# Kernel tuning notes

Measured on AMD Instinct MI355X. Metric: run time of the kernel, lower is better.

Reference implementation:

```python
import jax, jax.numpy as jnp
import numpy as np

EPS = 1e-12  # torch F.normalize eps

def _colnorm(w, g):
    # F.normalize(w, dim=0, p=2) * g  (column-wise L2 over dim 0)
    n = jnp.sqrt(jnp.sum(w * w, axis=0, keepdims=True))
    return (w / jnp.maximum(n, EPS)) * g

def setup_inputs() -> dict:
    key = jax.random.key(0)
    ks = jax.random.split(key, 16)
    B, T, V, E, H = 16, 512, 8192, 512, 1024
    inp = {
        'xs': jax.random.randint(ks[0], (B, T), 0, V),
        'ys': jax.random.randint(ks[1], (B, T), 0, V),
        'embed_w': jax.random.normal(ks[2], (V, E), jnp.float32) * 0.02,
        'wx': jax.random.normal(ks[3], (E, 4 * H), jnp.float32),
        'wh': jax.random.normal(ks[4], (H, 4 * H), jnp.float32),
        'wmx': jax.random.normal(ks[5], (E, H), jnp.float32),
        'wmh': jax.random.normal(ks[6], (H, H), jnp.float32),
        'b': jax.random.normal(ks[7], (4 * H,), jnp.float32) * 0.02,
        'gx': jax.random.normal(ks[8], (4 * H,), jnp.float32),
        'gh': jax.random.normal(ks[9], (4 * H,), jnp.float32),
        'gmx': jax.random.normal(ks[10], (H,), jnp.float32),
        'gmh': jax.random.normal(ks[11], (H,), jnp.float32),
        'pred_w': jax.random.normal(ks[12], (V, H), jnp.float32) * 0.02,
        'pred_b': jax.random.normal(ks[13], (V,), jnp.float32) * 0.02,
    }
    return inp

def reference(xs, ys, embed_w, wx, wh, wmx, wmh, b, gx, gh, gmx, gmh, pred_w, pred_b):
    B, T = xs.shape
    H = wmh.shape[0]
    V = pred_w.shape[0]
    # padding_idx=0 -> embedding row 0 is zero
    ew = embed_w.at[0].set(0.0)
    x = ew[xs]  # [B, T, E]
    # weight norm
    wx_n = _colnorm(wx, gx)
    wh_n = _colnorm(wh, gh)
    wmx_n = _colnorm(wmx, gmx)
    wmh_n = _colnorm(wmh, gmh)
    # precompute input-dependent projections (same math, batched over time)
    zx = jnp.einsum('bte,ef->btf', x, wx_n) + b     # [B, T, 4H]
    mx = jnp.einsum('bte,eh->bth', x, wmx_n)        # [B, T, H]

    def step(carry, inp):
        h, c = carry
        zx_t, mx_t = inp
        m = mx_t * (h @ wmh_n)                       # [B, H]
        z = zx_t + m @ wh_n                          # [B, 4H]
        i, f, o, u = jnp.split(z, 4, axis=1)
        i = jax.nn.sigmoid(i)
        f = jax.nn.sigmoid(f)
        o = jax.nn.sigmoid(o)
        u = jnp.tanh(u)
        c = f * c + i * u
        h = o * jnp.tanh(c)
        return (h, c), h

    h0 = jnp.zeros((B, H), x.dtype)
    c0 = jnp.zeros((B, H), x.dtype)
    _, hs = jax.lax.scan(step, (h0, c0), (zx.transpose(1, 0, 2), mx.transpose(1, 0, 2)))
    hs = hs.transpose(1, 0, 2)  # [B, T, H]
    logits = jnp.einsum('bth,vh->btv', hs, pred_w) + pred_b
    log_p = jax.nn.log_softmax(logits.reshape(B * T, V), axis=-1)
    nll = -jnp.take_along_axis(log_p, ys.reshape(B * T, 1), axis=1)
    return jnp.mean(nll)
```

## Files before the change

kernel.cpp:

```cpp
#include <hip/hip_runtime.h>
#include <hip/hip_bf16.h>
#include <stdint.h>

#define B_   16
#define T_   512
#define V_   8192
#define E_   512
#define H_   1024
#define BT_  (B_ * T_)
#define H4_  (4 * H_)

typedef __attribute__((ext_vector_type(8))) short   short8;
typedef __attribute__((ext_vector_type(8))) __bf16  bf16x8;
typedef __attribute__((ext_vector_type(4))) float   f32x4;
typedef __attribute__((ext_vector_type(4))) short   short4v;
typedef unsigned long long ull;

__device__ __forceinline__ float bf2f(short s) {
  union { unsigned u; float f; } x;
  x.u = ((unsigned)(unsigned short)s) << 16;
  return x.f;
}
__device__ __forceinline__ short f2bf(float f) {
  union { float f; unsigned u; } x; x.f = f;
  unsigned u = x.u;
  u = (u + 0x7fffu + ((u >> 16) & 1u)) >> 16;
  return (short)u;
}
__device__ __forceinline__ f32x4 mfma16(short8 a, short8 b, f32x4 c) {
  return __builtin_amdgcn_mfma_f32_16x16x32_bf16(
      __builtin_bit_cast(bf16x8, a), __builtin_bit_cast(bf16x8, b), c, 0, 0, 0);
}
__device__ __forceinline__ float sigm(float x) { return 1.f / (1.f + __expf(-x)); }
__device__ __forceinline__ float tanh_f(float x) { return 1.f - 2.f / (__expf(2.f * x) + 1.f); }

__device__ __forceinline__ short8 mk8(ull lo, ull hi) {
  union { ull u[2]; short8 s; } c;
  c.u[0] = lo; c.u[1] = hi;
  return c.s;
}

__global__ __launch_bounds__(256) void colscale(const float* __restrict__ W,
                                                const float* __restrict__ g,
                                                float* __restrict__ sc, int Kr, int N) {
  int j = blockIdx.x * 256 + threadIdx.x;
  if (j >= N) return;
  float ss = 0.f;
  for (int i = 0; i < Kr; ++i) { float v = W[(long)i * N + j]; ss = fmaf(v, v, ss); }
  sc[j] = g[j] / fmaxf(sqrtf(ss), 1e-12f);
}

__global__ __launch_bounds__(256) void transpose_cast(const float* __restrict__ W,
                                                      const float* __restrict__ sc,
                                                      short* __restrict__ WT, int Kr, int N) {
  __shared__ float tile[32][33];
  int nbi = Kr >> 5;
  int bi = blockIdx.x % nbi, bj = blockIdx.x / nbi;
  int i0 = bi << 5, j0 = bj << 5;
  int tx = threadIdx.x & 31, ty = threadIdx.x >> 5;
  for (int yy = ty; yy < 32; yy += 8)
    tile[yy][tx] = W[(long)(i0 + yy) * N + j0 + tx];
  __syncthreads();
  for (int yy = ty; yy < 32; yy += 8) {
    int j = j0 + yy;
    WT[(long)j * Kr + i0 + tx] = f2bf(tile[tx][yy] * sc[j]);
  }
}

__global__ __launch_bounds__(256) void castbf(const float* __restrict__ src,
                                              short* __restrict__ dst, long n) {
  long i = ((long)blockIdx.x * 256 + threadIdx.x) * 4;
  if (i + 3 < n) {
    float4 v = *(const float4*)(src + i);
    short4v o = { f2bf(v.x), f2bf(v.y), f2bf(v.z), f2bf(v.w) };
    *(short4v*)(dst + i) = o;
  }
}

__global__ __launch_bounds__(256) void embed_gather(const int* __restrict__ xs,
                                                    const float* __restrict__ ew,
                                                    short* __restrict__ x) {
  int r = blockIdx.x;
  int idx = xs[r];
  const float* src = ew + (long)idx * E_;
  for (int e = threadIdx.x; e < E_; e += 256) {
    float v = (idx == 0) ? 0.f : src[e];
    x[(long)r * E_ + e] = f2bf(v);
  }
}

__global__ __launch_bounds__(256) void gemm_bt(const short* __restrict__ A,
                                               const short* __restrict__ BT,
                                               const float* __restrict__ bias,
                                               short* __restrict__ C,
                                               int M, int N, int K) {
  int ntiles = N >> 7;
  int tM = (blockIdx.x / ntiles) << 7;
  int tN = (blockIdx.x % ntiles) << 7;
  int w = threadIdx.x >> 6, lane = threadIdx.x & 63;
  int mo = tM + ((w & 1) << 6), no = tN + ((w >> 1) << 6);
  int lr = lane & 15, lk8 = (lane >> 4) << 3, q = lane >> 4;
  f32x4 acc[4][4] = {};
  const short* Ap = A + (long)(mo + lr) * K + lk8;
  const short* Bp = BT + (long)(no + lr) * K + lk8;
  for (int k0 = 0; k0 < K; k0 += 32) {
    short8 af[4], bfr[4];
#pragma unroll
    for (int i = 0; i < 4; ++i) af[i] = *(const short8*)(Ap + (long)16 * i * K + k0);
#pragma unroll
    for (int j = 0; j < 4; ++j) bfr[j] = *(const short8*)(Bp + (long)16 * j * K + k0);
#pragma unroll
    for (int i = 0; i < 4; ++i)
#pragma unroll
      for (int j = 0; j < 4; ++j)
        acc[i][j] = mfma16(af[i], bfr[j], acc[i][j]);
  }
  float pbv[4];
#pragma unroll
  for (int j = 0; j < 4; ++j) pbv[j] = bias ? bias[no + 16 * j + lr] : 0.f;
#pragma unroll
  for (int i = 0; i < 4; ++i)
#pragma unroll
    for (int j = 0; j < 4; ++j)
#pragma unroll
      for (int r = 0; r < 4; ++r) {
        int row = mo + 16 * i + 4 * q + r;
        int col = no + 16 * j + lr;
        C[(long)row * N + col] = f2bf(acc[i][j][r] + pbv[j]);
      }
}

__global__ __launch_bounds__(256) void gemm_logits(const short* __restrict__ A,
                                                   const short* __restrict__ BT,
                                                   const float* __restrict__ pb,
                                                   const int* __restrict__ ys,
                                                   float* __restrict__ sumexp,
                                                   float* __restrict__ logit_y,
                                                   int M, int N, int K) {
  int ntiles = N >> 7;
  int tM = (blockIdx.x / ntiles) << 7;
  int tN = (blockIdx.x % ntiles) << 7;
  int w = threadIdx.x >> 6, lane = threadIdx.x & 63;
  int mo = tM + ((w & 1) << 6), no = tN + ((w >> 1) << 6);
  int lr = lane & 15, lk8 = (lane >> 4) << 3, q = lane >> 4;
  f32x4 acc[4][4] = {};
  const short* Ap = A + (long)(mo + lr) * K + lk8;
  const short* Bp = BT + (long)(no + lr) * K + lk8;
  for (int k0 = 0; k0 < K; k0 += 32) {
    short8 af[4], bfr[4];
#pragma unroll
    for (int i = 0; i < 4; ++i) af[i] = *(const short8*)(Ap + (long)16 * i * K + k0);
#pragma unroll
    for (int j = 0; j < 4; ++j) bfr[j] = *(const short8*)(Bp + (long)16 * j * K + k0);
#pragma unroll
    for (int i = 0; i < 4; ++i)
#pragma unroll
      for (int j = 0; j < 4; ++j)
        acc[i][j] = mfma16(af[i], bfr[j], acc[i][j]);
  }
  float pbv[4];
#pragma unroll
  for (int j = 0; j < 4; ++j) pbv[j] = pb[no + 16 * j + lr];
#pragma unroll
  for (int i = 0; i < 4; ++i) {
#pragma unroll
    for (int r = 0; r < 4; ++r) {
      int row = mo + 16 * i + 4 * q + r;
      int ysr = ys[row];
      float s = 0.f;
#pragma unroll
      for (int j = 0; j < 4; ++j) {
        float v = acc[i][j][r] + pbv[j];
        s += __expf(v);
        int col = no + 16 * j + lr;
        if (col == ysr) logit_y[row] = v;
      }
      s += __shfl_xor(s, 1); s += __shfl_xor(s, 2);
      s += __shfl_xor(s, 4); s += __shfl_xor(s, 8);
      if (lr == 0) atomicAdd(&sumexp[row], s);
    }
  }
}

#define NWG_ 64

__global__ __launch_bounds__(256, 1) void scan_kernel(
    const short* __restrict__ zxb, const short* __restrict__ mxb,
    const short* __restrict__ wmhT, const short* __restrict__ whT,
    short* __restrict__ hs,
    ull* __restrict__ h_prev,
    ull* __restrict__ m_buf,
    unsigned* __restrict__ flags_m,
    unsigned* __restrict__ flags_h) {
  const int g = blockIdx.x;
  const int tid = threadIdx.x;
  const int w = tid >> 6, lane = tid & 63;
  const int lr = lane & 15, q = lane >> 4;
  const int colg = g << 4;
  const int b = tid >> 4, cl = tid & 15;

  __shared__ float red1[4][16][16];
  __shared__ float red2[4][4][16][16];
  __shared__ __align__(8) short mtile[16][16];
  __shared__ __align__(8) short htile[16][16];

  short8 wmh_f[8];
#pragma unroll
  for (int kk = 0; kk < 8; ++kk) {
    const ull* p = (const ull*)(wmhT + (long)(colg + lr) * H_ + (w << 8) + (kk << 5) + (q << 3));
    ull lo = __hip_atomic_load(p, __ATOMIC_RELAXED, __HIP_MEMORY_SCOPE_WORKGROUP);
    ull hi = __hip_atomic_load(p + 1, __ATOMIC_RELAXED, __HIP_MEMORY_SCOPE_WORKGROUP);
    wmh_f[kk] = mk8(lo, hi);
  }
  short8 wh_f[4][8];
#pragma unroll
  for (int gt = 0; gt < 4; ++gt)
#pragma unroll
    for (int kk = 0; kk < 8; ++kk) {
      const ull* p = (const ull*)(whT + (long)(gt * H_ + colg + lr) * H_ + (w << 8) + (kk << 5) + (q << 3));
      ull lo = __hip_atomic_load(p, __ATOMIC_RELAXED, __HIP_MEMORY_SCOPE_WORKGROUP);
      ull hi = __hip_atomic_load(p + 1, __ATOMIC_RELAXED, __HIP_MEMORY_SCOPE_WORKGROUP);
      wh_f[gt][kk] = mk8(lo, hi);
    }

  float c = 0.f;
  const ull* hp = h_prev + lr * 256 + (w << 6) + (q << 1);
  const ull* mp = m_buf + lr * 256 + (w << 6) + (q << 1);

  for (int t = 0; t < T_; ++t) {
    long rrow = (long)(b * T_ + t);
    short mx_p = mxb[rrow * H_ + colg + cl];
    const short* zrow = zxb + rrow * H4_ + colg + cl;
    short z0p = zrow[0 * H_], z1p = zrow[1 * H_], z2p = zrow[2 * H_], z3p = zrow[3 * H_];

    if (tid < NWG_)
      while (__hip_atomic_load(&flags_h[tid << 5], __ATOMIC_RELAXED,
                               __HIP_MEMORY_SCOPE_AGENT) < (unsigned)t) {}
    __syncthreads();

    ull lh[16];
#pragma unroll
    for (int kk = 0; kk < 8; ++kk) {
      lh[2 * kk]     = __hip_atomic_load(hp + (kk << 3),     __ATOMIC_RELAXED, __HIP_MEMORY_SCOPE_AGENT);
      lh[2 * kk + 1] = __hip_atomic_load(hp + (kk << 3) + 1, __ATOMIC_RELAXED, __HIP_MEMORY_SCOPE_AGENT);
    }
    f32x4 a1 = {};
#pragma unroll
    for (int kk = 0; kk < 8; ++kk)
      a1 = mfma16(mk8(lh[2 * kk], lh[2 * kk + 1]), wmh_f[kk], a1);
#pragma unroll
    for (int r = 0; r < 4; ++r) red1[w][q * 4 + r][lr] = a1[r];
    __syncthreads();
    {
      float hw = red1[0][b][cl] + red1[1][b][cl] + red1[2][b][cl] + red1[3][b][cl];
      mtile[b][cl] = f2bf(bf2f(mx_p) * hw);
    }
    __syncthreads();
    if (tid < 64) {
      int b2 = tid >> 2, ch = tid & 3;
      ull v = *(const ull*)&mtile[b2][ch << 2];
      __hip_atomic_store(&m_buf[b2 * 256 + (colg >> 2) + ch], v,
                         __ATOMIC_RELAXED, __HIP_MEMORY_SCOPE_AGENT);
      __builtin_amdgcn_s_waitcnt(0);
      if (tid == 0)
        __hip_atomic_store(&flags_m[g << 5], (unsigned)(t + 1),
                           __ATOMIC_RELAXED, __HIP_MEMORY_SCOPE_AGENT);
    }

    if (tid < NWG_)
      while (__hip_atomic_load(&flags_m[tid << 5], __ATOMIC_RELAXED,
                               __HIP_MEMORY_SCOPE_AGENT) < (unsigned)(t + 1)) {}
    __syncthreads();

    ull lm[16];
#pragma unroll
    for (int kk = 0; kk < 8; ++kk) {
      lm[2 * kk]     = __hip_atomic_load(mp + (kk << 3),     __ATOMIC_RELAXED, __HIP_MEMORY_SCOPE_AGENT);
      lm[2 * kk + 1] = __hip_atomic_load(mp + (kk << 3) + 1, __ATOMIC_RELAXED, __HIP_MEMORY_SCOPE_AGENT);
    }
    f32x4 a2[4] = {};
#pragma unroll
    for (int kk = 0; kk < 8; ++kk) {
      short8 mf = mk8(lm[2 * kk], lm[2 * kk + 1]);
#pragma unroll
      for (int gt = 0; gt < 4; ++gt)
        a2[gt] = mfma16(mf, wh_f[gt][kk], a2[gt]);
    }
#pragma unroll
    for (int gt = 0; gt < 4; ++gt)
#pragma unroll
      for (int r = 0; r < 4; ++r)
        red2[w][gt][q * 4 + r][lr] = a2[gt][r];
    __syncthreads();
    {
      float zi = red2[0][0][b][cl] + red2[1][0][b][cl] + red2[2][0][b][cl] + red2[3][0][b][cl] + bf2f(z0p);
      float zf = red2[0][1][b][cl] + red2[1][1][b][cl] + red2[2][1][b][cl] + red2[3][1][b][cl] + bf2f(z1p);
      float zo = red2[0][2][b][cl] + red2[1][2][b][cl] + red2[2][2][b][cl] + red2[3][2][b][cl] + bf2f(z2p);
      float zu = red2[0][3][b][cl] + red2[1][3][b][cl] + red2[2][3][b][cl] + red2[3][3][b][cl] + bf2f(z3p);
      float ig = sigm(zi), fg = sigm(zf), og = sigm(zo), ug = tanh_f(zu);
      c = fg * c + ig * ug;
      float h = og * tanh_f(c);
      short hb = f2bf(h);
      htile[b][cl] = hb;
      hs[rrow * H_ + colg + cl] = hb;
    }
    __syncthreads();
    if (tid < 64) {
      int b2 = tid >> 2, ch = tid & 3;
      ull v = *(const ull*)&htile[b2][ch << 2];
      __hip_atomic_store(&h_prev[b2 * 256 + (colg >> 2) + ch], v,
                         __ATOMIC_RELAXED, __HIP_MEMORY_SCOPE_AGENT);
      __builtin_amdgcn_s_waitcnt(0);
      if (tid == 0)
        __hip_atomic_store(&flags_h[g << 5], (unsigned)(t + 1),
                           __ATOMIC_RELAXED, __HIP_MEMORY_SCOPE_AGENT);
    }
  }
}

__global__ __launch_bounds__(256) void reduce_nll(const float* __restrict__ se,
                                                  const float* __restrict__ ly,
                                                  float* __restrict__ out) {
  __shared__ float buf[256];
  float s = 0.f;
  for (int r = threadIdx.x; r < BT_; r += 256)
    s += logf(se[r]) - ly[r];
  buf[threadIdx.x] = s;
  __syncthreads();
  for (int off = 128; off > 0; off >>= 1) {
    if (threadIdx.x < off) buf[threadIdx.x] += buf[threadIdx.x + off];
    __syncthreads();
  }
  if (threadIdx.x == 0) out[0] = buf[0] * (1.0f / BT_);
}

extern "C" void kernel_launch(void* const* d_in, const int* in_sizes, int n_in,
                              void* d_out, int out_size, void* d_ws, size_t ws_size,
                              hipStream_t stream) {
  const int*   xs     = (const int*)d_in[0];
  const int*   ys     = (const int*)d_in[1];
  const float* embw   = (const float*)d_in[2];
  const float* wx     = (const float*)d_in[3];
  const float* wh     = (const float*)d_in[4];
  const float* wmx    = (const float*)d_in[5];
  const float* wmh    = (const float*)d_in[6];
  const float* bias   = (const float*)d_in[7];
  const float* gx     = (const float*)d_in[8];
  const float* gh     = (const float*)d_in[9];
  const float* gmx    = (const float*)d_in[10];
  const float* gmh    = (const float*)d_in[11];
  const float* pred_w = (const float*)d_in[12];
  const float* pred_b = (const float*)d_in[13];
  float* out = (float*)d_out;

  char* base = (char*)d_ws;
  size_t off = 0;
  auto alloc = [&](size_t bytes) -> void* {
    void* p = base + off;
    off = (off + bytes + 255) & ~(size_t)255;
    return p;
  };
  short* xb     = (short*)alloc((size_t)BT_ * E_ * 2);
  short* zxb    = (short*)alloc((size_t)BT_ * H4_ * 2);
  short* mxb    = (short*)alloc((size_t)BT_ * H_ * 2);
  short* hs     = (short*)alloc((size_t)BT_ * H_ * 2);
  short* wxT    = (short*)alloc((size_t)H4_ * E_ * 2);
  short* whT    = (short*)alloc((size_t)H4_ * H_ * 2);
  short* wmxT   = (short*)alloc((size_t)H_ * E_ * 2);
  short* wmhT   = (short*)alloc((size_t)H_ * H_ * 2);
  short* pwb    = (short*)alloc((size_t)V_ * H_ * 2);
  float* scx    = (float*)alloc(H4_ * 4);
  float* sch    = (float*)alloc(H4_ * 4);
  float* scmx   = (float*)alloc(H_ * 4);
  float* scmh   = (float*)alloc(H_ * 4);
  float* l_y    = (float*)alloc(BT_ * 4);
  ull*   m_buf  = (ull*)alloc(B_ * H_ * 2);
  size_t z0 = off;
  float*    sumexp  = (float*)alloc(BT_ * 4);
  unsigned* flags_m = (unsigned*)alloc(NWG_ * 32 * 4);
  unsigned* flags_h = (unsigned*)alloc(NWG_ * 32 * 4);
  ull*      h_prev  = (ull*)alloc(B_ * H_ * 2);
  size_t zlen = off - z0;

  hipMemsetAsync(base + z0, 0, zlen, stream);

  colscale<<<H4_ / 256, 256, 0, stream>>>(wx, gx, scx, E_, H4_);
  colscale<<<H4_ / 256, 256, 0, stream>>>(wh, gh, sch, H_, H4_);
  colscale<<<H_ / 256, 256, 0, stream>>>(wmx, gmx, scmx, E_, H_);
  colscale<<<H_ / 256, 256, 0, stream>>>(wmh, gmh, scmh, H_, H_);
  transpose_cast<<<(E_ / 32) * (H4_ / 32), 256, 0, stream>>>(wx, scx, wxT, E_, H4_);
  transpose_cast<<<(H_ / 32) * (H4_ / 32), 256, 0, stream>>>(wh, sch, whT, H_, H4_);
  transpose_cast<<<(E_ / 32) * (H_ / 32), 256, 0, stream>>>(wmx, scmx, wmxT, E_, H_);
  transpose_cast<<<(H_ / 32) * (H_ / 32), 256, 0, stream>>>(wmh, scmh, wmhT, H_, H_);
  castbf<<<((long)V_ * H_) / 1024, 256, 0, stream>>>(pred_w, pwb, (long)V_ * H_);

  embed_gather<<<BT_, 256, 0, stream>>>(xs, embw, xb);
  gemm_bt<<<(BT_ / 128) * (H4_ / 128), 256, 0, stream>>>(xb, wxT, bias, zxb, BT_, H4_, E_);
  gemm_bt<<<(BT_ / 128) * (H_ / 128), 256, 0, stream>>>(xb, wmxT, nullptr, mxb, BT_, H_, E_);

  scan_kernel<<<NWG_, 256, 0, stream>>>(zxb, mxb, wmhT, whT, hs,
                                        h_prev, m_buf, flags_m, flags_h);

  gemm_logits<<<(BT_ / 128) * (V_ / 128), 256, 0, stream>>>(hs, pwb, pred_b, ys,
                                                            sumexp, l_y, BT_, V_, H_);
  reduce_nll<<<1, 256, 0, stream>>>(sumexp, l_y, out);
}
```

Before: 5.774 ms.

## Replace flag-based cross-workgroup sync with step-tagged data words in scan

The scan kernel no longer publishes h and m through separate buffers guarded by per-workgroup flags. Each bf16 value is now stored in a 32-bit word whose upper 16 bits hold the step tag, and consumers spin on the data loads directly until every tag matches. This removes the flag poll, two __syncthreads per exchange, the LDS staging tile and the waitcnt before each flag store, cutting latency on the critical serial path. In exchange the exchange traffic doubles, each spin iteration reloads 32 words per lane, and the 16-bit tag limits the scheme to 65535 steps.

```diff
diff --git a/kernel.cpp b/kernel.cpp
--- a/kernel.cpp
+++ b/kernel.cpp
@@ -38,6 +38,17 @@
   union { ull u[2]; short8 s; } c;
   c.u[0] = lo; c.u[1] = hi;
   return c.s;
+}
+
+__device__ __forceinline__ short8 pack8(const ull* d) {
+  union { unsigned u[4]; short8 s; } r;
+#pragma unroll
+  for (int i = 0; i < 4; ++i) {
+    unsigned lo = (unsigned)d[i];
+    unsigned hi = (unsigned)(d[i] >> 32);
+    r.u[i] = (lo & 0xFFFFu) | (hi << 16);
+  }
+  return r.s;
 }
 
 __global__ __launch_bounds__(256) void colscale(const float* __restrict__ W,
@@ -188,10 +199,8 @@
     const short* __restrict__ zxb, const short* __restrict__ mxb,
     const short* __restrict__ wmhT, const short* __restrict__ whT,
     short* __restrict__ hs,
-    ull* __restrict__ h_prev,
-    ull* __restrict__ m_buf,
-    unsigned* __restrict__ flags_m,
-    unsigned* __restrict__ flags_h) {
+    unsigned* __restrict__ h_ex,
+    unsigned* __restrict__ m_ex) {
   const int g = blockIdx.x;
   const int tid = threadIdx.x;
   const int w = tid >> 6, lane = tid & 63;
@@ -201,8 +210,6 @@
 
   __shared__ float red1[4][16][16];
   __shared__ float red2[4][4][16][16];
-  __shared__ __align__(8) short mtile[16][16];
-  __shared__ __align__(8) short htile[16][16];
 
   short8 wmh_f[8];
 #pragma unroll
@@ -224,8 +231,10 @@
     }
 
   float c = 0.f;
-  const ull* hp = h_prev + lr * 256 + (w << 6) + (q << 1);
-  const ull* mp = m_buf + lr * 256 + (w << 6) + (q << 1);
+  const ull* hexp = (const ull*)h_ex + lr * 512 + (w << 7) + (q << 2);
+  const ull* mexp = (const ull*)m_ex + lr * 512 + (w << 7) + (q << 2);
+
+  ull d[32];
 
   for (int t = 0; t < T_; ++t) {
     long rrow = (long)(b * T_ + t);
@@ -233,55 +242,61 @@
     const short* zrow = zxb + rrow * H4_ + colg + cl;
     short z0p = zrow[0 * H_], z1p = zrow[1 * H_], z2p = zrow[2 * H_], z3p = zrow[3 * H_];
 
-    if (tid < NWG_)
-      while (__hip_atomic_load(&flags_h[tid << 5], __ATOMIC_RELAXED,
-                               __HIP_MEMORY_SCOPE_AGENT) < (unsigned)t) {}
-    __syncthreads();
-
-    ull lh[16];
-#pragma unroll
-    for (int kk = 0; kk < 8; ++kk) {
-      lh[2 * kk]     = __hip_atomic_load(hp + (kk << 3),     __ATOMIC_RELAXED, __HIP_MEMORY_SCOPE_AGENT);
-      lh[2 * kk + 1] = __hip_atomic_load(hp + (kk << 3) + 1, __ATOMIC_RELAXED, __HIP_MEMORY_SCOPE_AGENT);
+    {
+      const unsigned texp = (unsigned)t << 16;
+      for (;;) {
+#pragma unroll
+        for (int kk = 0; kk < 8; ++kk)
+#pragma unroll
+          for (int u = 0; u < 4; ++u)
+            d[(kk << 2) + u] = __hip_atomic_load(hexp + (kk << 4) + u,
+                                                 __ATOMIC_RELAXED, __HIP_MEMORY_SCOPE_AGENT);
+        unsigned bad = 0;
+#pragma unroll
+        for (int i2 = 0; i2 < 32; ++i2) {
+          bad |= ((unsigned)d[i2] ^ texp) & 0xFFFF0000u;
+          bad |= ((unsigned)(d[i2] >> 32) ^ texp) & 0xFFFF0000u;
+        }
+        if (bad == 0) break;
+      }
     }
     f32x4 a1 = {};
 #pragma unroll
     for (int kk = 0; kk < 8; ++kk)
-      a1 = mfma16(mk8(lh[2 * kk], lh[2 * kk + 1]), wmh_f[kk], a1);
+      a1 = mfma16(pack8(d + (kk << 2)), wmh_f[kk], a1);
 #pragma unroll
     for (int r = 0; r < 4; ++r) red1[w][q * 4 + r][lr] = a1[r];
     __syncthreads();
     {
       float hw = red1[0][b][cl] + red1[1][b][cl] + red1[2][b][cl] + red1[3][b][cl];
-      mtile[b][cl] = f2bf(bf2f(mx_p) * hw);
-    }
-    __syncthreads();
-    if (tid < 64) {
-      int b2 = tid >> 2, ch = tid & 3;
-      ull v = *(const ull*)&mtile[b2][ch << 2];
-      __hip_atomic_store(&m_buf[b2 * 256 + (colg >> 2) + ch], v,
+      short mv = f2bf(bf2f(mx_p) * hw);
+      __hip_atomic_store(&m_ex[(b << 10) + colg + cl],
+                         ((unsigned)(t + 1) << 16) | (unsigned)(unsigned short)mv,
                          __ATOMIC_RELAXED, __HIP_MEMORY_SCOPE_AGENT);
-      __builtin_amdgcn_s_waitcnt(0);
-      if (tid == 0)
-        __hip_atomic_store(&flags_m[g << 5], (unsigned)(t + 1),
-                           __ATOMIC_RELAXED, __HIP_MEMORY_SCOPE_AGENT);
-    }
-
-    if (tid < NWG_)
-      while (__hip_atomic_load(&flags_m[tid << 5], __ATOMIC_RELAXED,
-                               __HIP_MEMORY_SCOPE_AGENT) < (unsigned)(t + 1)) {}
-    __syncthreads();
-
-    ull lm[16];
+    }
+
+    {
+      const unsigned texp = (unsigned)(t + 1) << 16;
+      for (;;) {
+#pragma unroll
+        for (int kk = 0; kk < 8; ++kk)
+#pragma unroll
+          for (int u = 0; u < 4; ++u)
+            d[(kk << 2) + u] = __hip_atomic_load(mexp + (kk << 4) + u,
+                                                 __ATOMIC_RELAXED, __HIP_MEMORY_SCOPE_AGENT);
+        unsigned bad = 0;
+#pragma unroll
+        for (int i2 = 0; i2 < 32; ++i2) {
+          bad |= ((unsigned)d[i2] ^ texp) & 0xFFFF0000u;
+          bad |= ((unsigned)(d[i2] >> 32) ^ texp) & 0xFFFF0000u;
+        }
+        if (bad == 0) break;
+      }
+    }
+    f32x4 a2[4] = {};
 #pragma unroll
     for (int kk = 0; kk < 8; ++kk) {
-      lm[2 * kk]     = __hip_atomic_load(mp + (kk << 3),     __ATOMIC_RELAXED, __HIP_MEMORY_SCOPE_AGENT);
-      lm[2 * kk + 1] = __hip_atomic_load(mp + (kk << 3) + 1, __ATOMIC_RELAXED, __HIP_MEMORY_SCOPE_AGENT);
-    }
-    f32x4 a2[4] = {};
-#pragma unroll
-    for (int kk = 0; kk < 8; ++kk) {
-      short8 mf = mk8(lm[2 * kk], lm[2 * kk + 1]);
+      short8 mf = pack8(d + (kk << 2));
 #pragma unroll
       for (int gt = 0; gt < 4; ++gt)
         a2[gt] = mfma16(mf, wh_f[gt][kk], a2[gt]);
@@ -301,19 +316,10 @@
       c = fg * c + ig * ug;
       float h = og * tanh_f(c);
       short hb = f2bf(h);
-      htile[b][cl] = hb;
       hs[rrow * H_ + colg + cl] = hb;
-    }
-    __syncthreads();
-    if (tid < 64) {
-      int b2 = tid >> 2, ch = tid & 3;
-      ull v = *(const ull*)&htile[b2][ch << 2];
-      __hip_atomic_store(&h_prev[b2 * 256 + (colg >> 2) + ch], v,
+      __hip_atomic_store(&h_ex[(b << 10) + colg + cl],
+                         ((unsigned)(t + 1) << 16) | (unsigned)(unsigned short)hb,
                          __ATOMIC_RELAXED, __HIP_MEMORY_SCOPE_AGENT);
-      __builtin_amdgcn_s_waitcnt(0);
-      if (tid == 0)
-        __hip_atomic_store(&flags_h[g << 5], (unsigned)(t + 1),
-                           __ATOMIC_RELAXED, __HIP_MEMORY_SCOPE_AGENT);
     }
   }
 }
@@ -374,12 +380,10 @@
   float* scmx   = (float*)alloc(H_ * 4);
   float* scmh   = (float*)alloc(H_ * 4);
   float* l_y    = (float*)alloc(BT_ * 4);
-  ull*   m_buf  = (ull*)alloc(B_ * H_ * 2);
   size_t z0 = off;
-  float*    sumexp  = (float*)alloc(BT_ * 4);
-  unsigned* flags_m = (unsigned*)alloc(NWG_ * 32 * 4);
-  unsigned* flags_h = (unsigned*)alloc(NWG_ * 32 * 4);
-  ull*      h_prev  = (ull*)alloc(B_ * H_ * 2);
+  float*    sumexp = (float*)alloc(BT_ * 4);
+  unsigned* h_ex   = (unsigned*)alloc((size_t)B_ * H_ * 4);
+  unsigned* m_ex   = (unsigned*)alloc((size_t)B_ * H_ * 4);
   size_t zlen = off - z0;
 
   hipMemsetAsync(base + z0, 0, zlen, stream);
@@ -398,8 +402,7 @@
   gemm_bt<<<(BT_ / 128) * (H4_ / 128), 256, 0, stream>>>(xb, wxT, bias, zxb, BT_, H4_, E_);
   gemm_bt<<<(BT_ / 128) * (H_ / 128), 256, 0, stream>>>(xb, wmxT, nullptr, mxb, BT_, H_, E_);
 
-  scan_kernel<<<NWG_, 256, 0, stream>>>(zxb, mxb, wmhT, whT, hs,
-                                        h_prev, m_buf, flags_m, flags_h);
+  scan_kernel<<<NWG_, 256, 0, stream>>>(zxb, mxb, wmhT, whT, hs, h_ex, m_ex);
 
   gemm_logits<<<(BT_ / 128) * (V_ / 128), 256, 0, stream>>>(hs, pwb, pred_b, ys,
                                                             sumexp, l_y, BT_, V_, H_);
```

After: 9.065 ms. 57.0% more time.

## Replace block-wide barriers in scan with per-wave flag polling

Applied to the files above, without the earlier changes.

Drops the __syncthreads around each flag wait in the recurrent scan. Each lane now polls only the flag that guards the data it reads, and h flags are kept per wave instead of per workgroup. The staging through mtile/htile in shared memory and the barriers that went with it are removed: wave 0 reduces and writes m directly, and every wave packs h pairs with a shuffle and stores them itself. The aim is to shorten the critical path of each of the 512 sequential steps, at the cost of more flag traffic and more polling threads.

```diff
diff --git a/kernel.cpp b/kernel.cpp
--- a/kernel.cpp
+++ b/kernel.cpp
@@ -188,8 +188,8 @@
     const short* __restrict__ zxb, const short* __restrict__ mxb,
     const short* __restrict__ wmhT, const short* __restrict__ whT,
     short* __restrict__ hs,
-    ull* __restrict__ h_prev,
-    ull* __restrict__ m_buf,
+    ull* __restrict__ h_ex,
+    ull* __restrict__ m_ex,
     unsigned* __restrict__ flags_m,
     unsigned* __restrict__ flags_h) {
   const int g = blockIdx.x;
@@ -201,8 +201,6 @@
 
   __shared__ float red1[4][16][16];
   __shared__ float red2[4][4][16][16];
-  __shared__ __align__(8) short mtile[16][16];
-  __shared__ __align__(8) short htile[16][16];
 
   short8 wmh_f[8];
 #pragma unroll
@@ -224,19 +222,24 @@
     }
 
   float c = 0.f;
-  const ull* hp = h_prev + lr * 256 + (w << 6) + (q << 1);
-  const ull* mp = m_buf + lr * 256 + (w << 6) + (q << 1);
+  const ull* hp = h_ex + lr * 256 + (w << 6) + (q << 1);
+  const ull* mp = m_ex + lr * 256 + (w << 6) + (q << 1);
+  const unsigned* fh_poll = flags_h + (((w << 4) + (lane >> 2)) * 4 + (lane & 3)) * 16;
+  const unsigned* fm_poll = flags_m + ((w << 4) + lr) * 16;
+  const int b2 = tid >> 2, ch = tid & 3;
+  ull* m_st = m_ex + (b2 << 8) + (colg >> 2) + ch;
+  unsigned* h_st = (unsigned*)h_ex + (((b << 10) + colg + cl) >> 1);
 
   for (int t = 0; t < T_; ++t) {
     long rrow = (long)(b * T_ + t);
-    short mx_p = mxb[rrow * H_ + colg + cl];
     const short* zrow = zxb + rrow * H4_ + colg + cl;
     short z0p = zrow[0 * H_], z1p = zrow[1 * H_], z2p = zrow[2 * H_], z3p = zrow[3 * H_];
-
-    if (tid < NWG_)
-      while (__hip_atomic_load(&flags_h[tid << 5], __ATOMIC_RELAXED,
-                               __HIP_MEMORY_SCOPE_AGENT) < (unsigned)t) {}
-    __syncthreads();
+    ull mxq = 0;
+    if (w == 0)
+      mxq = *(const ull*)(mxb + (long)(b2 * T_ + t) * H_ + colg + (ch << 2));
+
+    while (__hip_atomic_load(fh_poll, __ATOMIC_RELAXED, __HIP_MEMORY_SCOPE_AGENT)
+           < (unsigned)t) {}
 
     ull lh[16];
 #pragma unroll
@@ -251,26 +254,25 @@
 #pragma unroll
     for (int r = 0; r < 4; ++r) red1[w][q * 4 + r][lr] = a1[r];
     __syncthreads();
-    {
-      float hw = red1[0][b][cl] + red1[1][b][cl] + red1[2][b][cl] + red1[3][b][cl];
-      mtile[b][cl] = f2bf(bf2f(mx_p) * hw);
-    }
-    __syncthreads();
-    if (tid < 64) {
-      int b2 = tid >> 2, ch = tid & 3;
-      ull v = *(const ull*)&mtile[b2][ch << 2];
-      __hip_atomic_store(&m_buf[b2 * 256 + (colg >> 2) + ch], v,
-                         __ATOMIC_RELAXED, __HIP_MEMORY_SCOPE_AGENT);
+
+    if (w == 0) {
+      union { short4v s; ull u; } pk;
+      union { short4v s; ull u; } mxu; mxu.u = mxq;
+#pragma unroll
+      for (int u = 0; u < 4; ++u) {
+        float s = red1[0][b2][(ch << 2) + u] + red1[1][b2][(ch << 2) + u] +
+                  red1[2][b2][(ch << 2) + u] + red1[3][b2][(ch << 2) + u];
+        pk.s[u] = f2bf(bf2f(mxu.s[u]) * s);
+      }
+      __hip_atomic_store(m_st, pk.u, __ATOMIC_RELAXED, __HIP_MEMORY_SCOPE_AGENT);
       __builtin_amdgcn_s_waitcnt(0);
       if (tid == 0)
-        __hip_atomic_store(&flags_m[g << 5], (unsigned)(t + 1),
+        __hip_atomic_store(&flags_m[g << 4], (unsigned)(t + 1),
                            __ATOMIC_RELAXED, __HIP_MEMORY_SCOPE_AGENT);
     }
 
-    if (tid < NWG_)
-      while (__hip_atomic_load(&flags_m[tid << 5], __ATOMIC_RELAXED,
-                               __HIP_MEMORY_SCOPE_AGENT) < (unsigned)(t + 1)) {}
-    __syncthreads();
+    while (__hip_atomic_load(fm_poll, __ATOMIC_RELAXED, __HIP_MEMORY_SCOPE_AGENT)
+           < (unsigned)(t + 1)) {}
 
     ull lm[16];
 #pragma unroll
@@ -292,6 +294,7 @@
       for (int r = 0; r < 4; ++r)
         red2[w][gt][q * 4 + r][lr] = a2[gt][r];
     __syncthreads();
+
     {
       float zi = red2[0][0][b][cl] + red2[1][0][b][cl] + red2[2][0][b][cl] + red2[3][0][b][cl] + bf2f(z0p);
       float zf = red2[0][1][b][cl] + red2[1][1][b][cl] + red2[2][1][b][cl] + red2[3][1][b][cl] + bf2f(z1p);
@@ -301,18 +304,15 @@
       c = fg * c + ig * ug;
       float h = og * tanh_f(c);
       short hb = f2bf(h);
-      htile[b][cl] = hb;
       hs[rrow * H_ + colg + cl] = hb;
-    }
-    __syncthreads();
-    if (tid < 64) {
-      int b2 = tid >> 2, ch = tid & 3;
-      ull v = *(const ull*)&htile[b2][ch << 2];
-      __hip_atomic_store(&h_prev[b2 * 256 + (colg >> 2) + ch], v,
-                         __ATOMIC_RELAXED, __HIP_MEMORY_SCOPE_AGENT);
+      unsigned hv = (unsigned)(unsigned short)hb;
+      unsigned ov = (unsigned)__shfl_xor((int)hv, 1);
+      if ((lane & 1) == 0)
+        __hip_atomic_store(h_st, hv | (ov << 16),
+                           __ATOMIC_RELAXED, __HIP_MEMORY_SCOPE_AGENT);
       __builtin_amdgcn_s_waitcnt(0);
-      if (tid == 0)
-        __hip_atomic_store(&flags_h[g << 5], (unsigned)(t + 1),
+      if (lane == 0)
+        __hip_atomic_store(&flags_h[((g << 2) + w) << 4], (unsigned)(t + 1),
                            __ATOMIC_RELAXED, __HIP_MEMORY_SCOPE_AGENT);
     }
   }
@@ -374,12 +374,12 @@
   float* scmx   = (float*)alloc(H_ * 4);
   float* scmh   = (float*)alloc(H_ * 4);
   float* l_y    = (float*)alloc(BT_ * 4);
-  ull*   m_buf  = (ull*)alloc(B_ * H_ * 2);
+  ull*   m_ex   = (ull*)alloc((size_t)B_ * H_ * 2);
   size_t z0 = off;
   float*    sumexp  = (float*)alloc(BT_ * 4);
-  unsigned* flags_m = (unsigned*)alloc(NWG_ * 32 * 4);
-  unsigned* flags_h = (unsigned*)alloc(NWG_ * 32 * 4);
-  ull*      h_prev  = (ull*)alloc(B_ * H_ * 2);
+  unsigned* flags_m = (unsigned*)alloc(NWG_ * 16 * 4);
+  unsigned* flags_h = (unsigned*)alloc(NWG_ * 4 * 16 * 4);
+  ull*      h_ex    = (ull*)alloc((size_t)B_ * H_ * 2);
   size_t zlen = off - z0;
 
   hipMemsetAsync(base + z0, 0, zlen, stream);
@@ -399,7 +399,7 @@
   gemm_bt<<<(BT_ / 128) * (H_ / 128), 256, 0, stream>>>(xb, wmxT, nullptr, mxb, BT_, H_, E_);
 
   scan_kernel<<<NWG_, 256, 0, stream>>>(zxb, mxb, wmhT, whT, hs,
-                                        h_prev, m_buf, flags_m, flags_h);
+                                        h_ex, m_ex, flags_m, flags_h);
 
   gemm_logits<<<(BT_ / 128) * (V_ / 128), 256, 0, stream>>>(hs, pwb, pred_b, ys,
                                                             sumexp, l_y, BT_, V_, H_);
```

New measurement: 5.862 ms. Within noise of the previous version (+1.5%).
